# Kernel tuning notes

Hardware: AMD Instinct MI355X
Metric: run time of the kernel (lower is better)

## Reference

```python
import jax, jax.numpy as jnp
import numpy as np

N, E, G = 50000, 400000, 2000
H, HEADS, HD = 128, 4, 32


def setup_inputs() -> dict:
    key = jax.random.key(0)
    ks = jax.random.split(key, 16)
    nrm = lambda k, shape, s=0.05: jax.random.normal(k, shape, dtype=jnp.float32) * s
    inp = {}
    inp["x"] = jax.random.normal(ks[0], (N, 39), dtype=jnp.float32)
    inp["edge_index"] = jax.random.randint(ks[1], (2, E), 0, N, dtype=jnp.int32)
    inp["edge_attr"] = jax.random.normal(ks[2], (E, 8), dtype=jnp.float32)
    inp["batch"] = jnp.sort(jax.random.randint(ks[3], (N,), 0, G, dtype=jnp.int32))
    inp["in_W"] = nrm(ks[4], (39, H)); inp["in_b"] = jnp.zeros((H,), jnp.float32)
    inp["in_g"] = jnp.ones((H,), jnp.float32); inp["in_beta"] = jnp.zeros((H,), jnp.float32)
    inp["Wl"] = nrm(ks[5], (3, H, H)); inp["Wr"] = nrm(ks[6], (3, H, H))
    inp["We"] = nrm(ks[7], (3, 8, H)); inp["att"] = nrm(ks[8], (3, HEADS, HD))
    inp["conv_b"] = jnp.zeros((3, H), jnp.float32)
    inp["bn_g"] = jnp.ones((3, H), jnp.float32); inp["bn_b"] = jnp.zeros((3, H), jnp.float32)
    inp["t1_W"] = nrm(ks[9], (3 * H, 256)); inp["t1_b"] = jnp.zeros((256,), jnp.float32)
    inp["t1_g"] = jnp.ones((256,), jnp.float32); inp["t1_beta"] = jnp.zeros((256,), jnp.float32)
    inp["t2_W"] = nrm(ks[10], (256, 128)); inp["t2_b"] = jnp.zeros((128,), jnp.float32)
    inp["t2_g"] = jnp.ones((128,), jnp.float32); inp["t2_beta"] = jnp.zeros((128,), jnp.float32)
    inp["head_W"] = nrm(ks[11], (128, 12)); inp["head_b"] = jnp.zeros((12,), jnp.float32)
    return inp


def _bn(h, g, b):
    # BatchNorm1d in training mode: normalize with batch statistics.
    m = h.mean(0)
    v = ((h - m) ** 2).mean(0)
    return g * (h - m) * jax.lax.rsqrt(v + 1e-5) + b


def reference(x, edge_index, edge_attr, batch, in_W, in_b, in_g, in_beta,
              Wl, Wr, We, att, conv_b, bn_g, bn_b,
              t1_W, t1_b, t1_g, t1_beta, t2_W, t2_b, t2_g, t2_beta,
              head_W, head_b):
    src, dst = edge_index[0], edge_index[1]  # messages flow src -> dst (PyG convention)
    xn = jax.nn.relu(_bn(x @ in_W + in_b, in_g, in_beta))  # [N, H]
    for l in range(3):  # three residual GATv2 layers
        xl = (xn @ Wl[l]).reshape(N, HEADS, HD)  # lin_l (source transform)
        xr = (xn @ Wr[l]).reshape(N, HEADS, HD)  # lin_r (target transform)
        ep = (edge_attr @ We[l]).reshape(E, HEADS, HD)
        m = jax.nn.leaky_relu(xl[src] + xr[dst] + ep, 0.2)  # [E, HEADS, HD]
        alpha = jnp.einsum('ehd,hd->eh', m, att[l])  # [E, HEADS]
        amax = jax.ops.segment_max(alpha, dst, num_segments=N)
        amax = jnp.where(jnp.isfinite(amax), amax, 0.0)  # nodes with no in-edges
        ae = jnp.exp(alpha - amax[dst])
        denom = jax.ops.segment_sum(ae, dst, num_segments=N)
        a = ae / (denom[dst] + 1e-16)  # scatter-softmax over neighborhoods
        agg = jax.ops.segment_sum(xl[src] * a[:, :, None], dst, num_segments=N)
        h = agg.reshape(N, H) + conv_b[l]
        h = jax.nn.elu(_bn(h, bn_g[l], bn_b[l]))
        xn = xn + h
    # 3-way global pooling per graph
    cnt = jax.ops.segment_sum(jnp.ones((N,), jnp.float32), batch, num_segments=G)
    sadd = jax.ops.segment_sum(xn, batch, num_segments=G)
    smean = sadd / jnp.maximum(cnt, 1.0)[:, None]
    smax = jax.ops.segment_max(xn, batch, num_segments=G)
    smax = jnp.where(cnt[:, None] > 0, smax, 0.0)
    xg = jnp.concatenate([smean, smax, sadd], axis=1)  # [G, 3H]
    t = jax.nn.relu(_bn(xg @ t1_W + t1_b, t1_g, t1_beta))
    t = jax.nn.relu(_bn(t @ t2_W + t2_b, t2_g, t2_beta))
    return jax.nn.sigmoid(t @ head_W + head_b)  # [G, 12]
```

## Files before the change

### kernel.cpp

```cpp
#include <hip/hip_runtime.h>
#include <math.h>


constexpr int N_ = 50000;
constexpr int E_ = 400000;
constexpr int G_ = 2000;
constexpr int H_ = 128;
constexpr int IN_ = 39;

__device__ __forceinline__ unsigned pk_bf16(float a, float b) {
  unsigned ua = __float_as_uint(a);
  unsigned ub = __float_as_uint(b);
  ua = (ua + 0x7fffu + ((ua >> 16) & 1u)) >> 16;
  ub = (ub + 0x7fffu + ((ub >> 16) & 1u)) & 0xffff0000u;
  return ua | ub;
}
__device__ __forceinline__ float up_lo(unsigned u) { return __uint_as_float(u << 16); }
__device__ __forceinline__ float up_hi(unsigned u) { return __uint_as_float(u & 0xffff0000u); }

__global__ __launch_bounds__(256) void hist_kernel(const int* __restrict__ keys, int n,
                                                   int* __restrict__ cnt) {
  for (int i = blockIdx.x * 256 + threadIdx.x; i < n; i += gridDim.x * 256)
    atomicAdd(&cnt[keys[i]], 1);
}

__global__ __launch_bounds__(1024) void scan_local(const int* __restrict__ in,
                                                   int* __restrict__ outx,
                                                   int* __restrict__ bsum, int n) {
  __shared__ int wsum[16];
  int t = threadIdx.x, lane = t & 63, wid = t >> 6;
  int idx = blockIdx.x * 1024 + t;
  int v = (idx < n) ? in[idx] : 0;
  int x = v;
#pragma unroll
  for (int off = 1; off < 64; off <<= 1) {
    int y = __shfl_up(x, off, 64);
    if (lane >= off) x += y;
  }
  if (lane == 63) wsum[wid] = x;
  __syncthreads();
  if (t == 0) {
    int acc = 0;
#pragma unroll
    for (int w = 0; w < 16; w++) { int tmp = wsum[w]; wsum[w] = acc; acc += tmp; }
    bsum[blockIdx.x] = acc;
  }
  __syncthreads();
  if (idx < n) outx[idx] = wsum[wid] + x - v;
}

__global__ __launch_bounds__(64) void scan_bsum(const int* __restrict__ bsum,
                                                int* __restrict__ boff, int nb) {
  int t = threadIdx.x;
  int v = (t < nb) ? bsum[t] : 0;
  int x = v;
#pragma unroll
  for (int off = 1; off < 64; off <<= 1) {
    int y = __shfl_up(x, off, 64);
    if (t >= off) x += y;
  }
  boff[t] = x - v;
}

__global__ __launch_bounds__(1024) void scan_add(int* __restrict__ eoff,
                                                 const int* __restrict__ boff,
                                                 int* __restrict__ cursor, int n) {
  int idx = blockIdx.x * 1024 + threadIdx.x;
  if (idx < n) {
    int e = eoff[idx] + boff[idx >> 10];
    eoff[idx] = e;
    cursor[idx] = e;
  }
  if (idx == 0) eoff[n] = E_;
}

__global__ __launch_bounds__(256) void goff_from_sorted(const int* __restrict__ batch,
                                                        int* __restrict__ goff) {
  int i = blockIdx.x * 256 + threadIdx.x;
  if (i >= N_) return;
  int bi = batch[i];
  int bp = (i == 0) ? -1 : batch[i - 1];
  for (int g = bp + 1; g <= bi; g++) goff[g] = i;
  if (i == N_ - 1) {
    for (int g = bi + 1; g <= G_; g++) goff[g] = N_;
  }
}

__global__ __launch_bounds__(256) void edge_scatter(const int* __restrict__ ei,
                                                    const float* __restrict__ ea,
                                                    int* __restrict__ cursor,
                                                    int* __restrict__ esrc,
                                                    unsigned* __restrict__ easb) {
  int e = blockIdx.x * 256 + threadIdx.x;
  if (e >= E_) return;
  int src = ei[e];
  int dst = ei[E_ + e];
  int j = atomicAdd(&cursor[dst], 1);
  esrc[j] = src;
  const float4* eav = (const float4*)(ea + (size_t)e * 8);
  float4 a0 = eav[0], a1 = eav[1];
  uint4 o;
  o.x = pk_bf16(a0.x, a0.y);
  o.y = pk_bf16(a0.z, a0.w);
  o.z = pk_bf16(a1.x, a1.y);
  o.w = pk_bf16(a1.z, a1.w);
  ((uint4*)easb)[j] = o;
}

__global__ __launch_bounds__(256) void in_gemm(const float* __restrict__ x,
                                               const float* __restrict__ W,
                                               const float* __restrict__ b,
                                               float* __restrict__ y,
                                               float* __restrict__ ssum,
                                               float* __restrict__ ssq) {
  __shared__ float xs[32][40];
  __shared__ float s1[256], s2[256];
  int t = threadIdx.x;
  int row0 = blockIdx.x * 32;
  for (int i = t; i < 32 * IN_; i += 256) {
    int r = i / IN_, k = i % IN_;
    int row = row0 + r;
    xs[r][k] = (row < N_) ? x[row * IN_ + k] : 0.f;
  }
  __syncthreads();
  int col = t & 127;
  int half = t >> 7;
  float acc[16];
#pragma unroll
  for (int r = 0; r < 16; r++) acc[r] = 0.f;
  for (int k = 0; k < IN_; k++) {
    float w = W[k * H_ + col];
#pragma unroll
    for (int r = 0; r < 16; r++) acc[r] = fmaf(xs[half * 16 + r][k], w, acc[r]);
  }
  float bb = b[col];
  float a1 = 0.f, a2 = 0.f;
#pragma unroll
  for (int r = 0; r < 16; r++) {
    int row = row0 + half * 16 + r;
    float v = acc[r] + bb;
    if (row < N_) {
      y[row * H_ + col] = v;
      a1 += v;
      a2 = fmaf(v, v, a2);
    }
  }
  s1[t] = a1; s2[t] = a2;
  __syncthreads();
  if (t < 128) {
    atomicAdd(&ssum[t], s1[t] + s1[t + 128]);
    atomicAdd(&ssq[t], s2[t] + s2[t + 128]);
  }
}

template <int MODE>
__global__ __launch_bounds__(256) void gemm_xlxr(const float* __restrict__ xn_ro,
                                                 float* __restrict__ xn,
                                                 const float* __restrict__ buf,
                                                 const float* __restrict__ g,
                                                 const float* __restrict__ beta,
                                                 const float* __restrict__ mean,
                                                 const float* __restrict__ rstd,
                                                 const float* __restrict__ Wlp,
                                                 const float* __restrict__ Wrp,
                                                 unsigned* __restrict__ xlb,
                                                 unsigned* __restrict__ xrb) {
  __shared__ float xs[64][16];
  __shared__ float wl_s[16][128];
  __shared__ float wr_s[16][128];
  int t = threadIdx.x;
  int tx = t & 31;
  int ty = t >> 5;
  int row0 = blockIdx.x * 64;
  float4 accl[8], accr[8];
#pragma unroll
  for (int r = 0; r < 8; r++) {
    accl[r] = make_float4(0.f, 0.f, 0.f, 0.f);
    accr[r] = make_float4(0.f, 0.f, 0.f, 0.f);
  }
  for (int kc = 0; kc < H_; kc += 16) {
    __syncthreads();
    {
      int r = t >> 2;
      int k4 = (t & 3) * 4;
      int row = row0 + r;
      int c = kc + k4;
      float4 v = make_float4(0.f, 0.f, 0.f, 0.f);
      if (row < N_) {
        if (MODE == 0) {
          v = *(const float4*)&xn_ro[row * H_ + c];
        } else {
          float4 bv = *(const float4*)&buf[row * H_ + c];
          float4 gv = *(const float4*)&g[c];
          float4 be = *(const float4*)&beta[c];
          float4 mn = *(const float4*)&mean[c];
          float4 rs = *(const float4*)&rstd[c];
          float t0 = gv.x * (bv.x - mn.x) * rs.x + be.x;
          float t1 = gv.y * (bv.y - mn.y) * rs.y + be.y;
          float t2 = gv.z * (bv.z - mn.z) * rs.z + be.z;
          float t3 = gv.w * (bv.w - mn.w) * rs.w + be.w;
          if (MODE == 1) {
            v = make_float4(fmaxf(t0, 0.f), fmaxf(t1, 0.f), fmaxf(t2, 0.f), fmaxf(t3, 0.f));
          } else {
            float4 xo = *(const float4*)&xn[row * H_ + c];
            v.x = xo.x + ((t0 > 0.f) ? t0 : (__expf(t0) - 1.f));
            v.y = xo.y + ((t1 > 0.f) ? t1 : (__expf(t1) - 1.f));
            v.z = xo.z + ((t2 > 0.f) ? t2 : (__expf(t2) - 1.f));
            v.w = xo.w + ((t3 > 0.f) ? t3 : (__expf(t3) - 1.f));
          }
          *(float4*)&xn[row * H_ + c] = v;
        }
      }
      *(float4*)&xs[r][k4] = v;
    }
    for (int i = t; i < 512; i += 256) {
      int k = i >> 5;
      int c4 = (i & 31) * 4;
      *(float4*)&wl_s[k][c4] = *(const float4*)&Wlp[(kc + k) * H_ + c4];
      *(float4*)&wr_s[k][c4] = *(const float4*)&Wrp[(kc + k) * H_ + c4];
    }
    __syncthreads();
#pragma unroll
    for (int k = 0; k < 16; k += 4) {
      float4 xv[8];
#pragma unroll
      for (int r = 0; r < 8; r++) xv[r] = *(const float4*)&xs[ty * 8 + r][k];
#pragma unroll
      for (int kk = 0; kk < 4; kk++) {
        float4 wl = *(const float4*)&wl_s[k + kk][tx * 4];
        float4 wr = *(const float4*)&wr_s[k + kk][tx * 4];
#pragma unroll
        for (int r = 0; r < 8; r++) {
          float xvr = (kk == 0) ? xv[r].x : (kk == 1) ? xv[r].y : (kk == 2) ? xv[r].z : xv[r].w;
          accl[r].x = fmaf(xvr, wl.x, accl[r].x);
          accl[r].y = fmaf(xvr, wl.y, accl[r].y);
          accl[r].z = fmaf(xvr, wl.z, accl[r].z);
          accl[r].w = fmaf(xvr, wl.w, accl[r].w);
          accr[r].x = fmaf(xvr, wr.x, accr[r].x);
          accr[r].y = fmaf(xvr, wr.y, accr[r].y);
          accr[r].z = fmaf(xvr, wr.z, accr[r].z);
          accr[r].w = fmaf(xvr, wr.w, accr[r].w);
        }
      }
    }
  }
#pragma unroll
  for (int r = 0; r < 8; r++) {
    int row = row0 + ty * 8 + r;
    if (row < N_) {
      uint2 ul, ur;
      ul.x = pk_bf16(accl[r].x, accl[r].y);
      ul.y = pk_bf16(accl[r].z, accl[r].w);
      ur.x = pk_bf16(accr[r].x, accr[r].y);
      ur.y = pk_bf16(accr[r].z, accr[r].w);
      *(uint2*)&xlb[(size_t)row * 64 + tx * 2] = ul;
      *(uint2*)&xrb[(size_t)row * 64 + tx * 2] = ur;
    }
  }
}

__device__ __forceinline__ float ep8u(const uint4& u, const float* w) {
  float ep = up_lo(u.x) * w[0];
  ep = fmaf(up_hi(u.x), w[1], ep);
  ep = fmaf(up_lo(u.y), w[2], ep);
  ep = fmaf(up_hi(u.y), w[3], ep);
  ep = fmaf(up_lo(u.z), w[4], ep);
  ep = fmaf(up_hi(u.z), w[5], ep);
  ep = fmaf(up_lo(u.w), w[6], ep);
  ep = fmaf(up_hi(u.w), w[7], ep);
  return ep;
}

__global__ __launch_bounds__(256) void agg_csr(const int* __restrict__ eoff,
                                               const int* __restrict__ esrc,
                                               const unsigned* __restrict__ easb,
                                               const float* __restrict__ Wel,
                                               const float* __restrict__ attl,
                                               const unsigned* __restrict__ xlb,
                                               const unsigned* __restrict__ xrb,
                                               const float* __restrict__ cb,
                                               float* __restrict__ buf,
                                               float* __restrict__ ssum,
                                               float* __restrict__ ssq) {
  __shared__ float sA[256], sB[256], sC[256], sD[256];
  int t = threadIdx.x;
  int l = t & 63;
  int sub = t >> 6;
  int c0 = l * 2;
  float w0[8], w1[8];
#pragma unroll
  for (int k = 0; k < 8; k++) {
    float2 wv = *(const float2*)&Wel[k * H_ + c0];
    w0[k] = wv.x; w1[k] = wv.y;
  }
  float2 attv = *(const float2*)&attl[c0];
  float2 cbv = *(const float2*)&cb[c0];
  const uint4* eas4 = (const uint4*)easb;
  float a1_0 = 0.f, a1_1 = 0.f, a2_0 = 0.f, a2_1 = 0.f;
  for (int n = blockIdx.x * 4 + sub; n < N_; n += gridDim.x * 4) {
    unsigned xru = xrb[(size_t)n * 64 + l];
    float xr0 = up_lo(xru), xr1 = up_hi(xru);
    int e0 = eoff[n], e1 = eoff[n + 1];
    float acc0 = 0.f, acc1 = 0.f, den = 0.f;
    int j = e0;
    for (; j + 4 <= e1; j += 4) {
      int s0 = esrc[j], s1 = esrc[j + 1], s2 = esrc[j + 2], s3 = esrc[j + 3];
      uint4 u0 = eas4[j], u1 = eas4[j + 1], u2 = eas4[j + 2], u3 = eas4[j + 3];
      unsigned xu0 = xlb[(size_t)s0 * 64 + l];
      unsigned xu1 = xlb[(size_t)s1 * 64 + l];
      unsigned xu2 = xlb[(size_t)s2 * 64 + l];
      unsigned xu3 = xlb[(size_t)s3 * 64 + l];
      float x00 = up_lo(xu0), x01 = up_hi(xu0);
      float x10 = up_lo(xu1), x11 = up_hi(xu1);
      float x20 = up_lo(xu2), x21 = up_hi(xu2);
      float x30 = up_lo(xu3), x31 = up_hi(xu3);
      float m00 = x00 + xr0 + ep8u(u0, w0);
      float m01 = x01 + xr1 + ep8u(u0, w1);
      float m10 = x10 + xr0 + ep8u(u1, w0);
      float m11 = x11 + xr1 + ep8u(u1, w1);
      float m20 = x20 + xr0 + ep8u(u2, w0);
      float m21 = x21 + xr1 + ep8u(u2, w1);
      float m30 = x30 + xr0 + ep8u(u3, w0);
      float m31 = x31 + xr1 + ep8u(u3, w1);
      m00 = (m00 > 0.f) ? m00 : 0.2f * m00;
      m01 = (m01 > 0.f) ? m01 : 0.2f * m01;
      m10 = (m10 > 0.f) ? m10 : 0.2f * m10;
      m11 = (m11 > 0.f) ? m11 : 0.2f * m11;
      m20 = (m20 > 0.f) ? m20 : 0.2f * m20;
      m21 = (m21 > 0.f) ? m21 : 0.2f * m21;
      m30 = (m30 > 0.f) ? m30 : 0.2f * m30;
      m31 = (m31 > 0.f) ? m31 : 0.2f * m31;
      float p0 = fmaf(m00, attv.x, m01 * attv.y);
      float p1 = fmaf(m10, attv.x, m11 * attv.y);
      float p2 = fmaf(m20, attv.x, m21 * attv.y);
      float p3 = fmaf(m30, attv.x, m31 * attv.y);
#pragma unroll
      for (int off = 8; off > 0; off >>= 1) {
        p0 += __shfl_xor(p0, off, 64);
        p1 += __shfl_xor(p1, off, 64);
        p2 += __shfl_xor(p2, off, 64);
        p3 += __shfl_xor(p3, off, 64);
      }
      float e0v = __expf(p0), e1v = __expf(p1), e2v = __expf(p2), e3v = __expf(p3);
      acc0 = fmaf(e0v, x00, acc0); acc1 = fmaf(e0v, x01, acc1);
      acc0 = fmaf(e1v, x10, acc0); acc1 = fmaf(e1v, x11, acc1);
      acc0 = fmaf(e2v, x20, acc0); acc1 = fmaf(e2v, x21, acc1);
      acc0 = fmaf(e3v, x30, acc0); acc1 = fmaf(e3v, x31, acc1);
      den += (e0v + e1v) + (e2v + e3v);
    }
    for (; j < e1; j++) {
      int s0 = esrc[j];
      uint4 u0 = eas4[j];
      unsigned xu0 = xlb[(size_t)s0 * 64 + l];
      float x00 = up_lo(xu0), x01 = up_hi(xu0);
      float m00 = x00 + xr0 + ep8u(u0, w0);
      float m01 = x01 + xr1 + ep8u(u0, w1);
      m00 = (m00 > 0.f) ? m00 : 0.2f * m00;
      m01 = (m01 > 0.f) ? m01 : 0.2f * m01;
      float p0 = fmaf(m00, attv.x, m01 * attv.y);
#pragma unroll
      for (int off = 8; off > 0; off >>= 1) p0 += __shfl_xor(p0, off, 64);
      float e0v = __expf(p0);
      acc0 = fmaf(e0v, x00, acc0);
      acc1 = fmaf(e0v, x01, acc1);
      den += e0v;
    }
    float inv = 1.f / (den + 1e-16f);
    float h0 = acc0 * inv + cbv.x;
    float h1 = acc1 * inv + cbv.y;
    *(float2*)&buf[(size_t)n * H_ + c0] = make_float2(h0, h1);
    a1_0 += h0; a1_1 += h1;
    a2_0 = fmaf(h0, h0, a2_0); a2_1 = fmaf(h1, h1, a2_1);
  }
  sA[t] = a1_0; sB[t] = a1_1; sC[t] = a2_0; sD[t] = a2_1;
  __syncthreads();
  if (t < 64) {
    float r1 = sA[t] + sA[t + 64] + sA[t + 128] + sA[t + 192];
    float r2 = sB[t] + sB[t + 64] + sB[t + 128] + sB[t + 192];
    float r3 = sC[t] + sC[t + 64] + sC[t + 128] + sC[t + 192];
    float r4 = sD[t] + sD[t + 64] + sD[t + 128] + sD[t + 192];
    atomicAdd(&ssum[2 * t], r1);
    atomicAdd(&ssum[2 * t + 1], r2);
    atomicAdd(&ssq[2 * t], r3);
    atomicAdd(&ssq[2 * t + 1], r4);
  }
}

__global__ void bn_final(float* __restrict__ ssum, float* __restrict__ ssq, float rows_inv,
                         int cols, float* __restrict__ mean, float* __restrict__ rstd) {
  int c = threadIdx.x;
  if (c < cols) {
    float m = ssum[c] * rows_inv;
    float v = ssq[c] * rows_inv - m * m;
    mean[c] = m;
    rstd[c] = rsqrtf(v + 1e-5f);
  }
  ssum[c] = 0.f;
  ssq[c] = 0.f;
}

__global__ __launch_bounds__(256) void apply_bn_relu(const float* __restrict__ y,
                                                     float* __restrict__ out,
                                                     const float* __restrict__ g,
                                                     const float* __restrict__ beta,
                                                     const float* __restrict__ mean,
                                                     const float* __restrict__ rstd,
                                                     long total, int cmask) {
  long i = (long)blockIdx.x * 256 + threadIdx.x;
  if (i >= total) return;
  int c = (int)i & cmask;
  float v = g[c] * (y[i] - mean[c]) * rstd[c] + beta[c];
  out[i] = fmaxf(v, 0.f);
}

__global__ __launch_bounds__(128) void pool_residual(const int* __restrict__ goff,
                                                     const float* __restrict__ xn,
                                                     const float* __restrict__ buf,
                                                     const float* __restrict__ g,
                                                     const float* __restrict__ beta,
                                                     const float* __restrict__ mean,
                                                     const float* __restrict__ rstd,
                                                     float* __restrict__ xg) {
  int gr = blockIdx.x;
  int t = threadIdx.x;
  int n0 = goff[gr], n1 = goff[gr + 1];
  float gg = g[t], bb = beta[t], mm = mean[t], rr = rstd[t];
  float s = 0.f, mx = -INFINITY;
  for (int n = n0; n < n1; n++) {
    float w = gg * (buf[(size_t)n * H_ + t] - mm) * rr + bb;
    w = (w > 0.f) ? w : (__expf(w) - 1.f);
    float v = xn[(size_t)n * H_ + t] + w;
    s += v;
    mx = fmaxf(mx, v);
  }
  float c = (float)(n1 - n0);
  xg[gr * 384 + t] = s / fmaxf(c, 1.f);
  xg[gr * 384 + 128 + t] = (c > 0.f) ? mx : 0.f;
  xg[gr * 384 + 256 + t] = s;
}

template <int K, int COLS>
__global__ void mlp_gemm(const float* __restrict__ A, const float* __restrict__ W,
                         const float* __restrict__ b, float* __restrict__ Y, int rows,
                         float* __restrict__ ssum, float* __restrict__ ssq) {
  __shared__ float xs[8][K];
  int t = threadIdx.x;
  int row0 = blockIdx.x * 8;
  for (int i = t; i < 8 * K; i += COLS) {
    int r = i / K, k = i % K;
    int row = row0 + r;
    xs[r][k] = (row < rows) ? A[row * K + k] : 0.f;
  }
  __syncthreads();
  float acc[8];
#pragma unroll
  for (int r = 0; r < 8; r++) acc[r] = 0.f;
  for (int k = 0; k < K; k++) {
    float w = W[k * COLS + t];
#pragma unroll
    for (int r = 0; r < 8; r++) acc[r] = fmaf(xs[r][k], w, acc[r]);
  }
  float bb = b[t];
  float a1 = 0.f, a2 = 0.f;
#pragma unroll
  for (int r = 0; r < 8; r++) {
    int row = row0 + r;
    if (row < rows) {
      float v = acc[r] + bb;
      Y[row * COLS + t] = v;
      a1 += v;
      a2 = fmaf(v, v, a2);
    }
  }
  atomicAdd(&ssum[t], a1);
  atomicAdd(&ssq[t], a2);
}

__global__ __launch_bounds__(64) void head_kernel(const float* __restrict__ u,
                                                  const float* __restrict__ W,
                                                  const float* __restrict__ b,
                                                  float* __restrict__ out) {
  __shared__ float row[128];
  int g = blockIdx.x;
  int t = threadIdx.x;
  row[t] = u[g * 128 + t];
  row[t + 64] = u[g * 128 + 64 + t];
  __syncthreads();
  if (t < 12) {
    float acc = b[t];
    for (int k = 0; k < 128; k++) acc = fmaf(row[k], W[k * 12 + t], acc);
    out[g * 12 + t] = 1.f / (1.f + expf(-acc));
  }
}

extern "C" void kernel_launch(void* const* d_in, const int* in_sizes, int n_in, void* d_out,
                              int out_size, void* d_ws, size_t ws_size, hipStream_t stream) {
  (void)in_sizes; (void)n_in; (void)out_size; (void)ws_size;
  const float* x       = (const float*)d_in[0];
  const int*   ei      = (const int*)d_in[1];
  const float* ea      = (const float*)d_in[2];
  const int*   batch   = (const int*)d_in[3];
  const float* in_W    = (const float*)d_in[4];
  const float* in_b    = (const float*)d_in[5];
  const float* in_g    = (const float*)d_in[6];
  const float* in_beta = (const float*)d_in[7];
  const float* Wl      = (const float*)d_in[8];
  const float* Wr      = (const float*)d_in[9];
  const float* We      = (const float*)d_in[10];
  const float* att     = (const float*)d_in[11];
  const float* conv_b  = (const float*)d_in[12];
  const float* bn_g    = (const float*)d_in[13];
  const float* bn_b    = (const float*)d_in[14];
  const float* t1_W    = (const float*)d_in[15];
  const float* t1_b    = (const float*)d_in[16];
  const float* t1_g    = (const float*)d_in[17];
  const float* t1_beta = (const float*)d_in[18];
  const float* t2_W    = (const float*)d_in[19];
  const float* t2_b    = (const float*)d_in[20];
  const float* t2_g    = (const float*)d_in[21];
  const float* t2_beta = (const float*)d_in[22];
  const float* head_W  = (const float*)d_in[23];
  const float* head_b  = (const float*)d_in[24];
  float* out = (float*)d_out;

  float* p = (float*)d_ws;
  float* xn   = p; p += N_ * H_;
  float* buf  = p; p += N_ * H_;
  float* ssum = p; p += 256;
  float* ssq  = p; p += 256;
  float* mean = p; p += 256;
  float* rstd = p; p += 256;
  float* xg   = p; p += G_ * 384;
  float* u1   = p; p += G_ * 256;
  float* u2   = p; p += G_ * 128;
  unsigned* up = (unsigned*)p;
  unsigned* xlb  = up; up += (size_t)N_ * 64;
  unsigned* xrb  = up; up += (size_t)N_ * 64;
  unsigned* easb = up; up += (size_t)E_ * 4;
  int* ip = (int*)up;
  int* deg    = ip; ip += N_;
  int* eoff   = ip; ip += N_ + 1;
  int* cursor = ip; ip += N_;
  int* goff   = ip; ip += G_ + 1;
  int* esrc   = ip; ip += E_;
  int* bsum   = ip; ip += 64;
  int* boff   = ip; ip += 64;

  hipMemsetAsync(deg, 0, (size_t)N_ * sizeof(int), stream);
  hist_kernel<<<1024, 256, 0, stream>>>(ei + E_, E_, deg);
  scan_local<<<49, 1024, 0, stream>>>(deg, eoff, bsum, N_);
  scan_bsum<<<1, 64, 0, stream>>>(bsum, boff, 49);
  scan_add<<<49, 1024, 0, stream>>>(eoff, boff, cursor, N_);
  edge_scatter<<<(E_ + 255) / 256, 256, 0, stream>>>(ei, ea, cursor, esrc, easb);
  goff_from_sorted<<<(N_ + 255) / 256, 256, 0, stream>>>(batch, goff);

  hipMemsetAsync(ssum, 0, 512 * sizeof(float), stream);
  in_gemm<<<(N_ + 31) / 32, 256, 0, stream>>>(x, in_W, in_b, buf, ssum, ssq);
  bn_final<<<1, 256, 0, stream>>>(ssum, ssq, 1.f / N_, H_, mean, rstd);

  for (int l = 0; l < 3; l++) {
    if (l == 0) {
      gemm_xlxr<1><<<(N_ + 63) / 64, 256, 0, stream>>>(xn, xn, buf, in_g, in_beta, mean, rstd,
                                                       Wl + l * H_ * H_, Wr + l * H_ * H_,
                                                       xlb, xrb);
    } else {
      gemm_xlxr<2><<<(N_ + 63) / 64, 256, 0, stream>>>(xn, xn, buf, bn_g + (l - 1) * H_,
                                                       bn_b + (l - 1) * H_, mean, rstd,
                                                       Wl + l * H_ * H_, Wr + l * H_ * H_,
                                                       xlb, xrb);
    }
    agg_csr<<<2048, 256, 0, stream>>>(eoff, esrc, easb, We + l * 8 * H_, att + l * H_,
                                      xlb, xrb, conv_b + l * H_, buf, ssum, ssq);
    bn_final<<<1, 256, 0, stream>>>(ssum, ssq, 1.f / N_, H_, mean, rstd);
  }

  pool_residual<<<G_, 128, 0, stream>>>(goff, xn, buf, bn_g + 2 * H_, bn_b + 2 * H_,
                                        mean, rstd, xg);

  mlp_gemm<384, 256><<<G_ / 8, 256, 0, stream>>>(xg, t1_W, t1_b, u1, G_, ssum, ssq);
  bn_final<<<1, 256, 0, stream>>>(ssum, ssq, 1.f / G_, 256, mean, rstd);
  apply_bn_relu<<<(G_ * 256 + 255) / 256, 256, 0, stream>>>(u1, u1, t1_g, t1_beta, mean, rstd,
                                                            (long)G_ * 256, 255);

  mlp_gemm<256, 128><<<G_ / 8, 128, 0, stream>>>(u1, t2_W, t2_b, u2, G_, ssum, ssq);
  bn_final<<<1, 256, 0, stream>>>(ssum, ssq, 1.f / G_, 128, mean, rstd);
  apply_bn_relu<<<(G_ * 128 + 255) / 256, 256, 0, stream>>>(u2, u2, t2_g, t2_beta, mean, rstd,
                                                            (long)G_ * 128, 127);

  head_kernel<<<G_, 64, 0, stream>>>(u2, head_W, head_b, out);
}
```

Baseline: 881.2 us.

## Sort nodes by degree and software-pipeline edge gathers in GAT aggregation

Adds a one-time counting sort of nodes by in-degree, so each wavefront processes nodes of similar degree and load imbalance between the wavefronts of a block drops. The aggregation loop now loads all source indices for a node at once into lanes and broadcasts them with shuffles. It double-buffers the next group of four xl rows and edge attributes while the current group is computed, and masks the tail instead of running a scalar remainder loop. It also sets launch bounds for higher occupancy and shrinks the grid, at the cost of extra setup kernels, more register pressure and padded over-reads of the edge-attribute array.

```diff
diff --git a/kernel.cpp b/kernel.cpp
--- a/kernel.cpp
+++ b/kernel.cpp
@@ -72,6 +72,35 @@
     cursor[idx] = e;
   }
   if (idx == 0) eoff[n] = E_;
+}
+
+__global__ __launch_bounds__(256) void deg_hist(const int* __restrict__ deg,
+                                                int* __restrict__ dcnt) {
+  int n = blockIdx.x * 256 + threadIdx.x;
+  if (n < N_) atomicAdd(&dcnt[min(deg[n], 63)], 1);
+}
+
+__global__ __launch_bounds__(64) void deg_scan(const int* __restrict__ dcnt,
+                                               int* __restrict__ dcur) {
+  int t = threadIdx.x;
+  int v = dcnt[t];
+  int x = v;
+#pragma unroll
+  for (int off = 1; off < 64; off <<= 1) {
+    int y = __shfl_up(x, off, 64);
+    if (t >= off) x += y;
+  }
+  dcur[t] = x - v;
+}
+
+__global__ __launch_bounds__(256) void deg_scatter(const int* __restrict__ deg,
+                                                   int* __restrict__ dcur,
+                                                   int* __restrict__ order) {
+  int n = blockIdx.x * 256 + threadIdx.x;
+  if (n < N_) {
+    int pos = atomicAdd(&dcur[min(deg[n], 63)], 1);
+    order[pos] = n;
+  }
 }
 
 __global__ __launch_bounds__(256) void goff_from_sorted(const int* __restrict__ batch,
@@ -271,17 +300,18 @@
   return ep;
 }
 
-__global__ __launch_bounds__(256) void agg_csr(const int* __restrict__ eoff,
-                                               const int* __restrict__ esrc,
-                                               const unsigned* __restrict__ easb,
-                                               const float* __restrict__ Wel,
-                                               const float* __restrict__ attl,
-                                               const unsigned* __restrict__ xlb,
-                                               const unsigned* __restrict__ xrb,
-                                               const float* __restrict__ cb,
-                                               float* __restrict__ buf,
-                                               float* __restrict__ ssum,
-                                               float* __restrict__ ssq) {
+__global__ __launch_bounds__(256, 5) void agg_csr(const int* __restrict__ order,
+                                                  const int* __restrict__ eoff,
+                                                  const int* __restrict__ esrc,
+                                                  const unsigned* __restrict__ easb,
+                                                  const float* __restrict__ Wel,
+                                                  const float* __restrict__ attl,
+                                                  const unsigned* __restrict__ xlb,
+                                                  const unsigned* __restrict__ xrb,
+                                                  const float* __restrict__ cb,
+                                                  float* __restrict__ buf,
+                                                  float* __restrict__ ssum,
+                                                  float* __restrict__ ssq) {
   __shared__ float sA[256], sB[256], sC[256], sD[256];
   int t = threadIdx.x;
   int l = t & 63;
@@ -297,73 +327,101 @@
   float2 cbv = *(const float2*)&cb[c0];
   const uint4* eas4 = (const uint4*)easb;
   float a1_0 = 0.f, a1_1 = 0.f, a2_0 = 0.f, a2_1 = 0.f;
-  for (int n = blockIdx.x * 4 + sub; n < N_; n += gridDim.x * 4) {
+  int stride = gridDim.x * 4;
+  for (int idx = blockIdx.x * 4 + sub; idx < N_; idx += stride) {
+    int n = order[idx];
     unsigned xru = xrb[(size_t)n * 64 + l];
     float xr0 = up_lo(xru), xr1 = up_hi(xru);
-    int e0 = eoff[n], e1 = eoff[n + 1];
+    int e0 = eoff[n];
+    int deg = eoff[n + 1] - e0;
     float acc0 = 0.f, acc1 = 0.f, den = 0.f;
-    int j = e0;
-    for (; j + 4 <= e1; j += 4) {
-      int s0 = esrc[j], s1 = esrc[j + 1], s2 = esrc[j + 2], s3 = esrc[j + 3];
-      uint4 u0 = eas4[j], u1 = eas4[j + 1], u2 = eas4[j + 2], u3 = eas4[j + 3];
-      unsigned xu0 = xlb[(size_t)s0 * 64 + l];
-      unsigned xu1 = xlb[(size_t)s1 * 64 + l];
-      unsigned xu2 = xlb[(size_t)s2 * 64 + l];
-      unsigned xu3 = xlb[(size_t)s3 * 64 + l];
-      float x00 = up_lo(xu0), x01 = up_hi(xu0);
-      float x10 = up_lo(xu1), x11 = up_hi(xu1);
-      float x20 = up_lo(xu2), x21 = up_hi(xu2);
-      float x30 = up_lo(xu3), x31 = up_hi(xu3);
-      float m00 = x00 + xr0 + ep8u(u0, w0);
-      float m01 = x01 + xr1 + ep8u(u0, w1);
-      float m10 = x10 + xr0 + ep8u(u1, w0);
-      float m11 = x11 + xr1 + ep8u(u1, w1);
-      float m20 = x20 + xr0 + ep8u(u2, w0);
-      float m21 = x21 + xr1 + ep8u(u2, w1);
-      float m30 = x30 + xr0 + ep8u(u3, w0);
-      float m31 = x31 + xr1 + ep8u(u3, w1);
-      m00 = (m00 > 0.f) ? m00 : 0.2f * m00;
-      m01 = (m01 > 0.f) ? m01 : 0.2f * m01;
-      m10 = (m10 > 0.f) ? m10 : 0.2f * m10;
-      m11 = (m11 > 0.f) ? m11 : 0.2f * m11;
-      m20 = (m20 > 0.f) ? m20 : 0.2f * m20;
-      m21 = (m21 > 0.f) ? m21 : 0.2f * m21;
-      m30 = (m30 > 0.f) ? m30 : 0.2f * m30;
-      m31 = (m31 > 0.f) ? m31 : 0.2f * m31;
-      float p0 = fmaf(m00, attv.x, m01 * attv.y);
-      float p1 = fmaf(m10, attv.x, m11 * attv.y);
-      float p2 = fmaf(m20, attv.x, m21 * attv.y);
-      float p3 = fmaf(m30, attv.x, m31 * attv.y);
-#pragma unroll
-      for (int off = 8; off > 0; off >>= 1) {
-        p0 += __shfl_xor(p0, off, 64);
-        p1 += __shfl_xor(p1, off, 64);
-        p2 += __shfl_xor(p2, off, 64);
-        p3 += __shfl_xor(p3, off, 64);
+    if (deg > 0 && deg <= 64) {
+      int s_all = (l < deg) ? esrc[e0 + l] : 0;
+      int C = (deg + 3) >> 2;
+      unsigned cx0, cx1, cx2, cx3;
+      uint4 cu0, cu1, cu2, cu3;
+      {
+        int s0 = __shfl(s_all, 0, 64), s1 = __shfl(s_all, 1, 64);
+        int s2 = __shfl(s_all, 2, 64), s3 = __shfl(s_all, 3, 64);
+        cu0 = eas4[e0 + 0]; cu1 = eas4[e0 + 1];
+        cu2 = eas4[e0 + 2]; cu3 = eas4[e0 + 3];
+        cx0 = xlb[(size_t)s0 * 64 + l]; cx1 = xlb[(size_t)s1 * 64 + l];
+        cx2 = xlb[(size_t)s2 * 64 + l]; cx3 = xlb[(size_t)s3 * 64 + l];
       }
-      float e0v = __expf(p0), e1v = __expf(p1), e2v = __expf(p2), e3v = __expf(p3);
-      acc0 = fmaf(e0v, x00, acc0); acc1 = fmaf(e0v, x01, acc1);
-      acc0 = fmaf(e1v, x10, acc0); acc1 = fmaf(e1v, x11, acc1);
-      acc0 = fmaf(e2v, x20, acc0); acc1 = fmaf(e2v, x21, acc1);
-      acc0 = fmaf(e3v, x30, acc0); acc1 = fmaf(e3v, x31, acc1);
-      den += (e0v + e1v) + (e2v + e3v);
-    }
-    for (; j < e1; j++) {
-      int s0 = esrc[j];
-      uint4 u0 = eas4[j];
-      unsigned xu0 = xlb[(size_t)s0 * 64 + l];
-      float x00 = up_lo(xu0), x01 = up_hi(xu0);
-      float m00 = x00 + xr0 + ep8u(u0, w0);
-      float m01 = x01 + xr1 + ep8u(u0, w1);
-      m00 = (m00 > 0.f) ? m00 : 0.2f * m00;
-      m01 = (m01 > 0.f) ? m01 : 0.2f * m01;
-      float p0 = fmaf(m00, attv.x, m01 * attv.y);
-#pragma unroll
-      for (int off = 8; off > 0; off >>= 1) p0 += __shfl_xor(p0, off, 64);
-      float e0v = __expf(p0);
-      acc0 = fmaf(e0v, x00, acc0);
-      acc1 = fmaf(e0v, x01, acc1);
-      den += e0v;
+      for (int c = 0; c < C; c++) {
+        unsigned nx0 = 0, nx1 = 0, nx2 = 0, nx3 = 0;
+        uint4 nu0 = make_uint4(0, 0, 0, 0), nu1 = nu0, nu2 = nu0, nu3 = nu0;
+        if (c + 1 < C) {
+          int jb = (c + 1) * 4;
+          int s0 = __shfl(s_all, jb + 0, 64), s1 = __shfl(s_all, jb + 1, 64);
+          int s2 = __shfl(s_all, jb + 2, 64), s3 = __shfl(s_all, jb + 3, 64);
+          nu0 = eas4[e0 + jb + 0]; nu1 = eas4[e0 + jb + 1];
+          nu2 = eas4[e0 + jb + 2]; nu3 = eas4[e0 + jb + 3];
+          nx0 = xlb[(size_t)s0 * 64 + l]; nx1 = xlb[(size_t)s1 * 64 + l];
+          nx2 = xlb[(size_t)s2 * 64 + l]; nx3 = xlb[(size_t)s3 * 64 + l];
+        }
+        int jb = c * 4;
+        float x00 = up_lo(cx0), x01 = up_hi(cx0);
+        float x10 = up_lo(cx1), x11 = up_hi(cx1);
+        float x20 = up_lo(cx2), x21 = up_hi(cx2);
+        float x30 = up_lo(cx3), x31 = up_hi(cx3);
+        float m00 = x00 + xr0 + ep8u(cu0, w0);
+        float m01 = x01 + xr1 + ep8u(cu0, w1);
+        float m10 = x10 + xr0 + ep8u(cu1, w0);
+        float m11 = x11 + xr1 + ep8u(cu1, w1);
+        float m20 = x20 + xr0 + ep8u(cu2, w0);
+        float m21 = x21 + xr1 + ep8u(cu2, w1);
+        float m30 = x30 + xr0 + ep8u(cu3, w0);
+        float m31 = x31 + xr1 + ep8u(cu3, w1);
+        m00 = (m00 > 0.f) ? m00 : 0.2f * m00;
+        m01 = (m01 > 0.f) ? m01 : 0.2f * m01;
+        m10 = (m10 > 0.f) ? m10 : 0.2f * m10;
+        m11 = (m11 > 0.f) ? m11 : 0.2f * m11;
+        m20 = (m20 > 0.f) ? m20 : 0.2f * m20;
+        m21 = (m21 > 0.f) ? m21 : 0.2f * m21;
+        m30 = (m30 > 0.f) ? m30 : 0.2f * m30;
+        m31 = (m31 > 0.f) ? m31 : 0.2f * m31;
+        float p0 = fmaf(m00, attv.x, m01 * attv.y);
+        float p1 = fmaf(m10, attv.x, m11 * attv.y);
+        float p2 = fmaf(m20, attv.x, m21 * attv.y);
+        float p3 = fmaf(m30, attv.x, m31 * attv.y);
+#pragma unroll
+        for (int off = 8; off > 0; off >>= 1) {
+          p0 += __shfl_xor(p0, off, 64);
+          p1 += __shfl_xor(p1, off, 64);
+          p2 += __shfl_xor(p2, off, 64);
+          p3 += __shfl_xor(p3, off, 64);
+        }
+        float e0v = (jb + 0 < deg) ? __expf(p0) : 0.f;
+        float e1v = (jb + 1 < deg) ? __expf(p1) : 0.f;
+        float e2v = (jb + 2 < deg) ? __expf(p2) : 0.f;
+        float e3v = (jb + 3 < deg) ? __expf(p3) : 0.f;
+        acc0 = fmaf(e0v, x00, acc0); acc1 = fmaf(e0v, x01, acc1);
+        acc0 = fmaf(e1v, x10, acc0); acc1 = fmaf(e1v, x11, acc1);
+        acc0 = fmaf(e2v, x20, acc0); acc1 = fmaf(e2v, x21, acc1);
+        acc0 = fmaf(e3v, x30, acc0); acc1 = fmaf(e3v, x31, acc1);
+        den += (e0v + e1v) + (e2v + e3v);
+        cx0 = nx0; cx1 = nx1; cx2 = nx2; cx3 = nx3;
+        cu0 = nu0; cu1 = nu1; cu2 = nu2; cu3 = nu3;
+      }
+    } else if (deg > 64) {
+      for (int j = e0; j < e0 + deg; j++) {
+        int s0 = esrc[j];
+        uint4 u0 = eas4[j];
+        unsigned xu0 = xlb[(size_t)s0 * 64 + l];
+        float x00 = up_lo(xu0), x01 = up_hi(xu0);
+        float m00 = x00 + xr0 + ep8u(u0, w0);
+        float m01 = x01 + xr1 + ep8u(u0, w1);
+        m00 = (m00 > 0.f) ? m00 : 0.2f * m00;
+        m01 = (m01 > 0.f) ? m01 : 0.2f * m01;
+        float p0 = fmaf(m00, attv.x, m01 * attv.y);
+#pragma unroll
+        for (int off = 8; off > 0; off >>= 1) p0 += __shfl_xor(p0, off, 64);
+        float e0v = __expf(p0);
+        acc0 = fmaf(e0v, x00, acc0);
+        acc1 = fmaf(e0v, x01, acc1);
+        den += e0v;
+      }
     }
     float inv = 1.f / (den + 1e-16f);
     float h0 = acc0 * inv + cbv.x;
@@ -536,21 +594,27 @@
   unsigned* up = (unsigned*)p;
   unsigned* xlb  = up; up += (size_t)N_ * 64;
   unsigned* xrb  = up; up += (size_t)N_ * 64;
-  unsigned* easb = up; up += (size_t)E_ * 4;
+  unsigned* easb = up; up += (size_t)E_ * 4 + 16;
   int* ip = (int*)up;
   int* deg    = ip; ip += N_;
+  int* dcnt   = ip; ip += 64;
   int* eoff   = ip; ip += N_ + 1;
   int* cursor = ip; ip += N_;
   int* goff   = ip; ip += G_ + 1;
   int* esrc   = ip; ip += E_;
   int* bsum   = ip; ip += 64;
   int* boff   = ip; ip += 64;
-
-  hipMemsetAsync(deg, 0, (size_t)N_ * sizeof(int), stream);
+  int* dcur   = ip; ip += 64;
+  int* order  = ip; ip += N_;
+
+  hipMemsetAsync(deg, 0, (size_t)(N_ + 64) * sizeof(int), stream);
   hist_kernel<<<1024, 256, 0, stream>>>(ei + E_, E_, deg);
   scan_local<<<49, 1024, 0, stream>>>(deg, eoff, bsum, N_);
   scan_bsum<<<1, 64, 0, stream>>>(bsum, boff, 49);
   scan_add<<<49, 1024, 0, stream>>>(eoff, boff, cursor, N_);
+  deg_hist<<<(N_ + 255) / 256, 256, 0, stream>>>(deg, dcnt);
+  deg_scan<<<1, 64, 0, stream>>>(dcnt, dcur);
+  deg_scatter<<<(N_ + 255) / 256, 256, 0, stream>>>(deg, dcur, order);
   edge_scatter<<<(E_ + 255) / 256, 256, 0, stream>>>(ei, ea, cursor, esrc, easb);
   goff_from_sorted<<<(N_ + 255) / 256, 256, 0, stream>>>(batch, goff);
 
@@ -569,7 +633,7 @@
                                                        Wl + l * H_ * H_, Wr + l * H_ * H_,
                                                        xlb, xrb);
     }
-    agg_csr<<<2048, 256, 0, stream>>>(eoff, esrc, easb, We + l * 8 * H_, att + l * H_,
+    agg_csr<<<1280, 256, 0, stream>>>(order, eoff, esrc, easb, We + l * 8 * H_, att + l * H_,
                                       xlb, xrb, conv_b + l * H_, buf, ssum, ssq);
     bn_final<<<1, 256, 0, stream>>>(ssum, ssq, 1.f / N_, H_, mean, rstd);
   }
```

New measurement: 1.551 ms. 1.76x slower.

## Use bf16 MFMA for per-layer projections and fold BN finalize into consumers

Applied to the files above, without the earlier changes.

Replaces the fp32 FMA tiled GEMM for the lin_l/lin_r projections with bf16 MFMA 16x16x32 instructions. The normalized activation tile is staged in LDS as bf16 and the weights are transposed to bf16 on each load. It also removes the separate bn_final kernels: each BN stage gets its own zeroed sum/sumsq slot, and consumers compute mean and rstd inline. This cuts kernel launches and scalar FMA work, at the cost of bf16 rounding of the GEMM inputs and redundant per-thread rsqrt computations.

```diff
diff --git a/kernel.cpp b/kernel.cpp
--- a/kernel.cpp
+++ b/kernel.cpp
@@ -7,6 +7,9 @@
 constexpr int G_ = 2000;
 constexpr int H_ = 128;
 constexpr int IN_ = 39;
+
+typedef __attribute__((ext_vector_type(8))) short bf16x8;
+typedef __attribute__((ext_vector_type(4))) float f32x4;
 
 __device__ __forceinline__ unsigned pk_bf16(float a, float b) {
   unsigned ua = __float_as_uint(a);
@@ -14,6 +17,11 @@
   ua = (ua + 0x7fffu + ((ua >> 16) & 1u)) >> 16;
   ub = (ub + 0x7fffu + ((ub >> 16) & 1u)) & 0xffff0000u;
   return ua | ub;
+}
+__device__ __forceinline__ unsigned short bf16_1(float x) {
+  unsigned u = __float_as_uint(x);
+  u = (u + 0x7fffu + ((u >> 16) & 1u)) >> 16;
+  return (unsigned short)u;
 }
 __device__ __forceinline__ float up_lo(unsigned u) { return __uint_as_float(u << 16); }
 __device__ __forceinline__ float up_hi(unsigned u) { return __uint_as_float(u & 0xffff0000u); }
@@ -154,108 +162,117 @@
 }
 
 template <int MODE>
-__global__ __launch_bounds__(256) void gemm_xlxr(const float* __restrict__ xn_ro,
-                                                 float* __restrict__ xn,
+__global__ __launch_bounds__(256) void gemm_mfma(float* __restrict__ xn,
                                                  const float* __restrict__ buf,
                                                  const float* __restrict__ g,
                                                  const float* __restrict__ beta,
-                                                 const float* __restrict__ mean,
-                                                 const float* __restrict__ rstd,
+                                                 const float* __restrict__ ssum,
+                                                 const float* __restrict__ ssq,
+                                                 float rows_inv,
                                                  const float* __restrict__ Wlp,
                                                  const float* __restrict__ Wrp,
                                                  unsigned* __restrict__ xlb,
                                                  unsigned* __restrict__ xrb) {
-  __shared__ float xs[64][16];
-  __shared__ float wl_s[16][128];
-  __shared__ float wr_s[16][128];
+  __shared__ char smem[17408 + 20480];
+  short (*a_s)[136] = (short(*)[136])smem;
+  short (*b_s)[40] = (short(*)[40])(smem + 17408);
+  float* t2base = (float*)(smem + 17408);
   int t = threadIdx.x;
-  int tx = t & 31;
-  int ty = t >> 5;
+  int lane = t & 63, w = t >> 6;
+  int quad = lane >> 4, lc = lane & 15;
   int row0 = blockIdx.x * 64;
-  float4 accl[8], accr[8];
-#pragma unroll
-  for (int r = 0; r < 8; r++) {
-    accl[r] = make_float4(0.f, 0.f, 0.f, 0.f);
-    accr[r] = make_float4(0.f, 0.f, 0.f, 0.f);
-  }
-  for (int kc = 0; kc < H_; kc += 16) {
+
+  {
+    int r = t >> 2;
+    int row = row0 + r;
+    int kb0 = (t & 3) * 32;
+    bool valid = row < N_;
+    for (int kk = 0; kk < 32; kk += 4) {
+      int c = kb0 + kk;
+      float4 v = make_float4(0.f, 0.f, 0.f, 0.f);
+      if (valid) {
+        float4 bv = *(const float4*)&buf[(size_t)row * H_ + c];
+        float4 gv = *(const float4*)&g[c];
+        float4 be = *(const float4*)&beta[c];
+        float4 s1 = *(const float4*)&ssum[c];
+        float4 s2 = *(const float4*)&ssq[c];
+        float m0 = s1.x * rows_inv, m1 = s1.y * rows_inv, m2 = s1.z * rows_inv, m3 = s1.w * rows_inv;
+        float r0 = rsqrtf(s2.x * rows_inv - m0 * m0 + 1e-5f);
+        float r1 = rsqrtf(s2.y * rows_inv - m1 * m1 + 1e-5f);
+        float r2 = rsqrtf(s2.z * rows_inv - m2 * m2 + 1e-5f);
+        float r3 = rsqrtf(s2.w * rows_inv - m3 * m3 + 1e-5f);
+        float t0 = gv.x * (bv.x - m0) * r0 + be.x;
+        float t1 = gv.y * (bv.y - m1) * r1 + be.y;
+        float t2 = gv.z * (bv.z - m2) * r2 + be.z;
+        float t3 = gv.w * (bv.w - m3) * r3 + be.w;
+        if (MODE == 1) {
+          v = make_float4(fmaxf(t0, 0.f), fmaxf(t1, 0.f), fmaxf(t2, 0.f), fmaxf(t3, 0.f));
+        } else {
+          float4 xo = *(const float4*)&xn[(size_t)row * H_ + c];
+          v.x = xo.x + ((t0 > 0.f) ? t0 : (__expf(t0) - 1.f));
+          v.y = xo.y + ((t1 > 0.f) ? t1 : (__expf(t1) - 1.f));
+          v.z = xo.z + ((t2 > 0.f) ? t2 : (__expf(t2) - 1.f));
+          v.w = xo.w + ((t3 > 0.f) ? t3 : (__expf(t3) - 1.f));
+        }
+        *(float4*)&xn[(size_t)row * H_ + c] = v;
+      }
+      uint2 pk;
+      pk.x = pk_bf16(v.x, v.y);
+      pk.y = pk_bf16(v.z, v.w);
+      *(uint2*)&a_s[r][c] = pk;
+    }
+  }
+
+  f32x4 acc[16];
+#pragma unroll
+  for (int nt = 0; nt < 16; nt++) acc[nt] = (f32x4){0.f, 0.f, 0.f, 0.f};
+
+  for (int kb = 0; kb < 4; kb++) {
     __syncthreads();
-    {
-      int r = t >> 2;
-      int k4 = (t & 3) * 4;
-      int row = row0 + r;
-      int c = kc + k4;
-      float4 v = make_float4(0.f, 0.f, 0.f, 0.f);
-      if (row < N_) {
-        if (MODE == 0) {
-          v = *(const float4*)&xn_ro[row * H_ + c];
-        } else {
-          float4 bv = *(const float4*)&buf[row * H_ + c];
-          float4 gv = *(const float4*)&g[c];
-          float4 be = *(const float4*)&beta[c];
-          float4 mn = *(const float4*)&mean[c];
-          float4 rs = *(const float4*)&rstd[c];
-          float t0 = gv.x * (bv.x - mn.x) * rs.x + be.x;
-          float t1 = gv.y * (bv.y - mn.y) * rs.y + be.y;
-          float t2 = gv.z * (bv.z - mn.z) * rs.z + be.z;
-          float t3 = gv.w * (bv.w - mn.w) * rs.w + be.w;
-          if (MODE == 1) {
-            v = make_float4(fmaxf(t0, 0.f), fmaxf(t1, 0.f), fmaxf(t2, 0.f), fmaxf(t3, 0.f));
-          } else {
-            float4 xo = *(const float4*)&xn[row * H_ + c];
-            v.x = xo.x + ((t0 > 0.f) ? t0 : (__expf(t0) - 1.f));
-            v.y = xo.y + ((t1 > 0.f) ? t1 : (__expf(t1) - 1.f));
-            v.z = xo.z + ((t2 > 0.f) ? t2 : (__expf(t2) - 1.f));
-            v.w = xo.w + ((t3 > 0.f) ? t3 : (__expf(t3) - 1.f));
-          }
-          *(float4*)&xn[row * H_ + c] = v;
-        }
+    for (int i = t; i < 2048; i += 256) {
+      int k_local = i >> 6;
+      int n4 = (i & 63) << 2;
+      const float* Wsrc = (n4 < 128) ? Wlp : Wrp;
+      int nn = (n4 < 128) ? n4 : n4 - 128;
+      float4 wv = *(const float4*)&Wsrc[(kb * 32 + k_local) * H_ + nn];
+      b_s[n4 + 0][k_local] = bf16_1(wv.x);
+      b_s[n4 + 1][k_local] = bf16_1(wv.y);
+      b_s[n4 + 2][k_local] = bf16_1(wv.z);
+      b_s[n4 + 3][k_local] = bf16_1(wv.w);
+    }
+    __syncthreads();
+    bf16x8 av = *(const bf16x8*)&a_s[w * 16 + lc][kb * 32 + quad * 8];
+#pragma unroll
+    for (int nt = 0; nt < 16; nt++) {
+      bf16x8 bv = *(const bf16x8*)&b_s[nt * 16 + lc][quad * 8];
+      acc[nt] = __builtin_amdgcn_mfma_f32_16x16x32_bf16(av, bv, acc[nt], 0, 0, 0);
+    }
+  }
+  __syncthreads();
+
+  float* t2 = t2base + w * 544;
+  for (int ntp = 0; ntp < 8; ntp++) {
+#pragma unroll
+    for (int rr = 0; rr < 4; rr++) {
+      t2[(quad * 4 + rr) * 34 + lc] = acc[2 * ntp][rr];
+      t2[(quad * 4 + rr) * 34 + 16 + lc] = acc[2 * ntp + 1][rr];
+    }
+    __asm__ volatile("s_waitcnt lgkmcnt(0)" ::: "memory");
+#pragma unroll
+    for (int it = 0; it < 4; it++) {
+      int item = lane + it * 64;
+      int p = item & 15, rowi = item >> 4;
+      float v0 = t2[rowi * 34 + 2 * p];
+      float v1 = t2[rowi * 34 + 2 * p + 1];
+      unsigned u = pk_bf16(v0, v1);
+      int colpair = ntp * 16 + p;
+      int rowg = row0 + w * 16 + rowi;
+      if (rowg < N_) {
+        if (colpair < 64) xlb[(size_t)rowg * 64 + colpair] = u;
+        else xrb[(size_t)rowg * 64 + colpair - 64] = u;
       }
-      *(float4*)&xs[r][k4] = v;
-    }
-    for (int i = t; i < 512; i += 256) {
-      int k = i >> 5;
-      int c4 = (i & 31) * 4;
-      *(float4*)&wl_s[k][c4] = *(const float4*)&Wlp[(kc + k) * H_ + c4];
-      *(float4*)&wr_s[k][c4] = *(const float4*)&Wrp[(kc + k) * H_ + c4];
-    }
-    __syncthreads();
-#pragma unroll
-    for (int k = 0; k < 16; k += 4) {
-      float4 xv[8];
-#pragma unroll
-      for (int r = 0; r < 8; r++) xv[r] = *(const float4*)&xs[ty * 8 + r][k];
-#pragma unroll
-      for (int kk = 0; kk < 4; kk++) {
-        float4 wl = *(const float4*)&wl_s[k + kk][tx * 4];
-        float4 wr = *(const float4*)&wr_s[k + kk][tx * 4];
-#pragma unroll
-        for (int r = 0; r < 8; r++) {
-          float xvr = (kk == 0) ? xv[r].x : (kk == 1) ? xv[r].y : (kk == 2) ? xv[r].z : xv[r].w;
-          accl[r].x = fmaf(xvr, wl.x, accl[r].x);
-          accl[r].y = fmaf(xvr, wl.y, accl[r].y);
-          accl[r].z = fmaf(xvr, wl.z, accl[r].z);
-          accl[r].w = fmaf(xvr, wl.w, accl[r].w);
-          accr[r].x = fmaf(xvr, wr.x, accr[r].x);
-          accr[r].y = fmaf(xvr, wr.y, accr[r].y);
-          accr[r].z = fmaf(xvr, wr.z, accr[r].z);
-          accr[r].w = fmaf(xvr, wr.w, accr[r].w);
-        }
-      }
-    }
-  }
-#pragma unroll
-  for (int r = 0; r < 8; r++) {
-    int row = row0 + ty * 8 + r;
-    if (row < N_) {
-      uint2 ul, ur;
-      ul.x = pk_bf16(accl[r].x, accl[r].y);
-      ul.y = pk_bf16(accl[r].z, accl[r].w);
-      ur.x = pk_bf16(accr[r].x, accr[r].y);
-      ur.y = pk_bf16(accr[r].z, accr[r].w);
-      *(uint2*)&xlb[(size_t)row * 64 + tx * 2] = ul;
-      *(uint2*)&xrb[(size_t)row * 64 + tx * 2] = ur;
-    }
+    }
+    __asm__ volatile("s_waitcnt lgkmcnt(0)" ::: "memory");
   }
 }
 
@@ -386,30 +403,20 @@
   }
 }
 
-__global__ void bn_final(float* __restrict__ ssum, float* __restrict__ ssq, float rows_inv,
-                         int cols, float* __restrict__ mean, float* __restrict__ rstd) {
-  int c = threadIdx.x;
-  if (c < cols) {
-    float m = ssum[c] * rows_inv;
-    float v = ssq[c] * rows_inv - m * m;
-    mean[c] = m;
-    rstd[c] = rsqrtf(v + 1e-5f);
-  }
-  ssum[c] = 0.f;
-  ssq[c] = 0.f;
-}
-
 __global__ __launch_bounds__(256) void apply_bn_relu(const float* __restrict__ y,
                                                      float* __restrict__ out,
                                                      const float* __restrict__ g,
                                                      const float* __restrict__ beta,
-                                                     const float* __restrict__ mean,
-                                                     const float* __restrict__ rstd,
+                                                     const float* __restrict__ ssum,
+                                                     const float* __restrict__ ssq,
+                                                     float rows_inv,
                                                      long total, int cmask) {
   long i = (long)blockIdx.x * 256 + threadIdx.x;
   if (i >= total) return;
   int c = (int)i & cmask;
-  float v = g[c] * (y[i] - mean[c]) * rstd[c] + beta[c];
+  float m = ssum[c] * rows_inv;
+  float rs = rsqrtf(ssq[c] * rows_inv - m * m + 1e-5f);
+  float v = g[c] * (y[i] - m) * rs + beta[c];
   out[i] = fmaxf(v, 0.f);
 }
 
@@ -418,13 +425,16 @@
                                                      const float* __restrict__ buf,
                                                      const float* __restrict__ g,
                                                      const float* __restrict__ beta,
-                                                     const float* __restrict__ mean,
-                                                     const float* __restrict__ rstd,
+                                                     const float* __restrict__ ssum,
+                                                     const float* __restrict__ ssq,
+                                                     float rows_inv,
                                                      float* __restrict__ xg) {
   int gr = blockIdx.x;
   int t = threadIdx.x;
   int n0 = goff[gr], n1 = goff[gr + 1];
-  float gg = g[t], bb = beta[t], mm = mean[t], rr = rstd[t];
+  float mm = ssum[t] * rows_inv;
+  float rr = rsqrtf(ssq[t] * rows_inv - mm * mm + 1e-5f);
+  float gg = g[t], bb = beta[t];
   float s = 0.f, mx = -INFINITY;
   for (int n = n0; n < n1; n++) {
     float w = gg * (buf[(size_t)n * H_ + t] - mm) * rr + bb;
@@ -524,15 +534,12 @@
   float* out = (float*)d_out;
 
   float* p = (float*)d_ws;
-  float* xn   = p; p += N_ * H_;
-  float* buf  = p; p += N_ * H_;
-  float* ssum = p; p += 256;
-  float* ssq  = p; p += 256;
-  float* mean = p; p += 256;
-  float* rstd = p; p += 256;
-  float* xg   = p; p += G_ * 384;
-  float* u1   = p; p += G_ * 256;
-  float* u2   = p; p += G_ * 128;
+  float* xn    = p; p += N_ * H_;
+  float* buf   = p; p += N_ * H_;
+  float* sstat = p; p += 6 * 512;
+  float* xg    = p; p += G_ * 384;
+  float* u1    = p; p += G_ * 256;
+  float* u2    = p; p += G_ * 128;
   unsigned* up = (unsigned*)p;
   unsigned* xlb  = up; up += (size_t)N_ * 64;
   unsigned* xrb  = up; up += (size_t)N_ * 64;
@@ -546,7 +553,11 @@
   int* bsum   = ip; ip += 64;
   int* boff   = ip; ip += 64;
 
+#define SSUM(s) (sstat + (s) * 512)
+#define SSQ(s)  (sstat + (s) * 512 + 256)
+
   hipMemsetAsync(deg, 0, (size_t)N_ * sizeof(int), stream);
+  hipMemsetAsync(sstat, 0, 6 * 512 * sizeof(float), stream);
   hist_kernel<<<1024, 256, 0, stream>>>(ei + E_, E_, deg);
   scan_local<<<49, 1024, 0, stream>>>(deg, eoff, bsum, N_);
   scan_bsum<<<1, 64, 0, stream>>>(bsum, boff, 49);
@@ -554,38 +565,37 @@
   edge_scatter<<<(E_ + 255) / 256, 256, 0, stream>>>(ei, ea, cursor, esrc, easb);
   goff_from_sorted<<<(N_ + 255) / 256, 256, 0, stream>>>(batch, goff);
 
-  hipMemsetAsync(ssum, 0, 512 * sizeof(float), stream);
-  in_gemm<<<(N_ + 31) / 32, 256, 0, stream>>>(x, in_W, in_b, buf, ssum, ssq);
-  bn_final<<<1, 256, 0, stream>>>(ssum, ssq, 1.f / N_, H_, mean, rstd);
-
+  in_gemm<<<(N_ + 31) / 32, 256, 0, stream>>>(x, in_W, in_b, buf, SSUM(0), SSQ(0));
+
+  const float rnInv = 1.f / N_;
   for (int l = 0; l < 3; l++) {
     if (l == 0) {
-      gemm_xlxr<1><<<(N_ + 63) / 64, 256, 0, stream>>>(xn, xn, buf, in_g, in_beta, mean, rstd,
-                                                       Wl + l * H_ * H_, Wr + l * H_ * H_,
-                                                       xlb, xrb);
+      gemm_mfma<1><<<782, 256, 0, stream>>>(xn, buf, in_g, in_beta, SSUM(0), SSQ(0), rnInv,
+                                            Wl + l * H_ * H_, Wr + l * H_ * H_, xlb, xrb);
     } else {
-      gemm_xlxr<2><<<(N_ + 63) / 64, 256, 0, stream>>>(xn, xn, buf, bn_g + (l - 1) * H_,
-                                                       bn_b + (l - 1) * H_, mean, rstd,
-                                                       Wl + l * H_ * H_, Wr + l * H_ * H_,
-                                                       xlb, xrb);
+      gemm_mfma<2><<<782, 256, 0, stream>>>(xn, buf, bn_g + (l - 1) * H_, bn_b + (l - 1) * H_,
+                                            SSUM(l), SSQ(l), rnInv,
+                                            Wl + l * H_ * H_, Wr + l * H_ * H_, xlb, xrb);
     }
     agg_csr<<<2048, 256, 0, stream>>>(eoff, esrc, easb, We + l * 8 * H_, att + l * H_,
-                                      xlb, xrb, conv_b + l * H_, buf, ssum, ssq);
-    bn_final<<<1, 256, 0, stream>>>(ssum, ssq, 1.f / N_, H_, mean, rstd);
+                                      xlb, xrb, conv_b + l * H_, buf, SSUM(l + 1), SSQ(l + 1));
   }
 
   pool_residual<<<G_, 128, 0, stream>>>(goff, xn, buf, bn_g + 2 * H_, bn_b + 2 * H_,
-                                        mean, rstd, xg);
-
-  mlp_gemm<384, 256><<<G_ / 8, 256, 0, stream>>>(xg, t1_W, t1_b, u1, G_, ssum, ssq);
-  bn_final<<<1, 256, 0, stream>>>(ssum, ssq, 1.f / G_, 256, mean, rstd);
-  apply_bn_relu<<<(G_ * 256 + 255) / 256, 256, 0, stream>>>(u1, u1, t1_g, t1_beta, mean, rstd,
+                                        SSUM(3), SSQ(3), rnInv, xg);
+
+  const float rgInv = 1.f / G_;
+  mlp_gemm<384, 256><<<G_ / 8, 256, 0, stream>>>(xg, t1_W, t1_b, u1, G_, SSUM(4), SSQ(4));
+  apply_bn_relu<<<(G_ * 256 + 255) / 256, 256, 0, stream>>>(u1, u1, t1_g, t1_beta,
+                                                            SSUM(4), SSQ(4), rgInv,
                                                             (long)G_ * 256, 255);
 
-  mlp_gemm<256, 128><<<G_ / 8, 128, 0, stream>>>(u1, t2_W, t2_b, u2, G_, ssum, ssq);
-  bn_final<<<1, 256, 0, stream>>>(ssum, ssq, 1.f / G_, 128, mean, rstd);
-  apply_bn_relu<<<(G_ * 128 + 255) / 256, 256, 0, stream>>>(u2, u2, t2_g, t2_beta, mean, rstd,
+  mlp_gemm<256, 128><<<G_ / 8, 128, 0, stream>>>(u1, t2_W, t2_b, u2, G_, SSUM(5), SSQ(5));
+  apply_bn_relu<<<(G_ * 128 + 255) / 256, 256, 0, stream>>>(u2, u2, t2_g, t2_beta,
+                                                            SSUM(5), SSQ(5), rgInv,
                                                             (long)G_ * 128, 127);
 
   head_kernel<<<G_, 64, 0, stream>>>(u2, head_W, head_b, out);
-}
+#undef SSUM
+#undef SSQ
+}
```

After: 915.3 us. +3.9%, slower.
